# Kernel optimization log

Hardware: AMD Instinct MI355X
Metric: run time of the kernel (lower is better)

The kernel has to match this reference:

```python
import jax, jax.numpy as jnp
import numpy as np

EPS = 1e-5

def layer_norm(x, gamma):
    mu = jnp.mean(x, axis=-1, keepdims=True)
    var = jnp.mean(jnp.square(x - mu), axis=-1, keepdims=True)
    return (x - mu) / jnp.sqrt(var + EPS) * gamma

def setup_inputs() -> dict:
    key = jax.random.key(0)
    ks = jax.random.split(key, 10)
    b, n, j = 2, 2048, 2048
    dim, ctx_dim, heads, dim_head, ff_mult = 1024, 1024, 16, 64, 4
    inner = heads * dim_head
    ff_inner = ff_mult * dim
    s = 0.02
    return {
        'x': jax.random.normal(ks[0], (b, n, dim), jnp.float32),
        'context': jax.random.normal(ks[1], (b, j, ctx_dim), jnp.float32),
        'mask': jax.random.randint(ks[2], (b, j), 0, 2, jnp.int32),
        'gamma': jnp.ones((dim,), jnp.float32),
        'ctx_gamma': jnp.ones((ctx_dim,), jnp.float32),
        'Wq': jax.random.normal(ks[3], (dim, inner), jnp.float32) * s,
        'Wkv': jax.random.normal(ks[4], (ctx_dim, 2 * dim_head), jnp.float32) * s,
        'Wout': jax.random.normal(ks[5], (inner, dim), jnp.float32) * s,
        'Wff1': jax.random.normal(ks[6], (dim, 2 * ff_inner), jnp.float32) * s,
        'Wff2': jax.random.normal(ks[7], (ff_inner, dim), jnp.float32) * s,
    }

def reference(x, context, mask, gamma, ctx_gamma, Wq, Wkv, Wout, Wff1, Wff2):
    heads, dim_head = 16, 64
    b, n, dim = x.shape
    scale = dim_head ** -0.5
    xn = layer_norm(x, gamma)                              # [b,n,dim]
    ctx = layer_norm(context, ctx_gamma)                   # [b,j,cd]
    q = (xn @ Wq).reshape(b, n, heads, dim_head).transpose(0, 2, 1, 3) * scale  # [b,h,n,d]
    kv = ctx @ Wkv                                         # [b,j,2d]
    k, v = kv[..., :dim_head], kv[..., dim_head:]          # [b,j,d] each (multi-query)
    sim = jnp.einsum('bhid,bjd->bhij', q, k)               # [b,h,n,j]
    sim = jnp.where((mask == 0)[:, None, None, :], -jnp.inf, sim)
    attn = jax.nn.softmax(sim, axis=-1)
    out = jnp.einsum('bhij,bjd->bhid', attn, v)            # [b,h,n,d]
    out = out.transpose(0, 2, 1, 3).reshape(b, n, heads * dim_head)
    out = out @ Wout                                       # [b,n,dim]
    # parallel SwiGLU FF on normalized x
    h = xn @ Wff1
    ff_inner = Wff2.shape[0]
    a, gate = h[..., :ff_inner], h[..., ff_inner:]
    out = out + (jax.nn.silu(gate) * a) @ Wff2
    return out
```

## Files before the change

### kernel.cpp

```cpp
#include <hip/hip_runtime.h>

typedef unsigned short u16;
typedef unsigned int   u32;
typedef __bf16  bf16x8 __attribute__((ext_vector_type(8)));
typedef __bf16  bf16x2 __attribute__((ext_vector_type(2)));
typedef float   f32x4  __attribute__((ext_vector_type(4)));

static __device__ __forceinline__ float b2f(u16 v) {
    return __builtin_bit_cast(float, (u32)(((u32)v) << 16));
}
static __device__ __forceinline__ u16 f2b(float f) {
    u32 u = __builtin_bit_cast(u32, f);
    return (u16)((u + 0x7FFFu + ((u >> 16) & 1u)) >> 16);
}
static __device__ __forceinline__ u32 pack2(float a, float b) {
    bf16x2 t; t[0] = (__bf16)a; t[1] = (__bf16)b;
    return __builtin_bit_cast(u32, t);
}

__global__ __launch_bounds__(256)
void ln_kernel(const float* __restrict__ x, const float* __restrict__ ctx,
               const float* __restrict__ gamma, const float* __restrict__ cgamma,
               u16* __restrict__ xn, u16* __restrict__ ctxn)
{
    const int row = blockIdx.x;
    const int tid = threadIdx.x;
    const float* src; const float* g; u16* dst;
    if (row < 4096) { src = x   + (long)row * 1024;          g = gamma;  dst = xn   + (long)row * 1024; }
    else            { src = ctx + (long)(row - 4096) * 1024; g = cgamma; dst = ctxn + (long)(row - 4096) * 1024; }
    float4 v = ((const float4*)src)[tid];
    float s = v.x + v.y + v.z + v.w;
    float q = v.x*v.x + v.y*v.y + v.z*v.z + v.w*v.w;
#pragma unroll
    for (int off = 32; off; off >>= 1) { s += __shfl_xor(s, off); q += __shfl_xor(q, off); }
    __shared__ float r1[4], r2[4];
    if ((tid & 63) == 0) { r1[tid >> 6] = s; r2[tid >> 6] = q; }
    __syncthreads();
    s = r1[0] + r1[1] + r1[2] + r1[3];
    q = r2[0] + r2[1] + r2[2] + r2[3];
    float mu   = s * (1.0f / 1024.0f);
    float var  = q * (1.0f / 1024.0f) - mu * mu;
    float rstd = rsqrtf(var + 1e-5f);
    float4 gv = ((const float4*)g)[tid];
    ushort4 o;
    o.x = f2b((v.x - mu) * rstd * gv.x);
    o.y = f2b((v.y - mu) * rstd * gv.y);
    o.z = f2b((v.z - mu) * rstd * gv.z);
    o.w = f2b((v.w - mu) * rstd * gv.w);
    ((ushort4*)dst)[tid] = o;
}

__global__ __launch_bounds__(256)
void wconv(const float* __restrict__ W, u16* __restrict__ Wt, int N, int K, float scale)
{
    __shared__ float tile[32][33];
    const int tid = threadIdx.x;
    const int n0 = blockIdx.x * 32;
    const int k0 = blockIdx.y * 32;
    const int r  = tid >> 3;
    const int c4 = (tid & 7) * 4;
    float4 v = *(const float4*)&W[(long)(k0 + r) * N + n0 + c4];
    tile[r][c4 + 0] = v.x; tile[r][c4 + 1] = v.y; tile[r][c4 + 2] = v.z; tile[r][c4 + 3] = v.w;
    __syncthreads();
    ushort4 o;
    o.x = f2b(tile[c4 + 0][r] * scale);
    o.y = f2b(tile[c4 + 1][r] * scale);
    o.z = f2b(tile[c4 + 2][r] * scale);
    o.w = f2b(tile[c4 + 3][r] * scale);
    *(ushort4*)&Wt[(long)(n0 + r) * K + k0 + c4] = o;
}

__global__ __launch_bounds__(256)
void wconv_ff1(const float* __restrict__ W, u16* __restrict__ Wt)
{
    __shared__ float tile[32][33];
    const int tid = threadIdx.x;
    const int a  = blockIdx.x;
    const int k0 = blockIdx.y * 32;
    const int r  = tid >> 3;
    const int c4 = (tid & 7) * 4;
    const int srccol = (c4 < 16) ? (a * 16 + c4) : (4096 + a * 16 + (c4 - 16));
    float4 v = *(const float4*)&W[(long)(k0 + r) * 8192 + srccol];
    tile[r][c4 + 0] = v.x; tile[r][c4 + 1] = v.y; tile[r][c4 + 2] = v.z; tile[r][c4 + 3] = v.w;
    __syncthreads();
    ushort4 o;
    o.x = f2b(tile[c4 + 0][r]);
    o.y = f2b(tile[c4 + 1][r]);
    o.z = f2b(tile[c4 + 2][r]);
    o.w = f2b(tile[c4 + 3][r]);
    *(ushort4*)&Wt[(long)(a * 32 + r) * 1024 + k0 + c4] = o;
}

__global__ __launch_bounds__(256)
void kext_build(const float* __restrict__ kvf, const int* __restrict__ mask,
                u16* __restrict__ kext, float* __restrict__ mbias)
{
    const int gid = blockIdx.x * 256 + threadIdx.x;
    const int b = gid >> 14;
    const int rem = gid & 16383;
    const int j = rem >> 3;
    const int c = rem & 7;
    const float* src = &kvf[((long)b * 2048 + j) * 128 + c * 8];
    u16 ov[8];
#pragma unroll
    for (int e = 0; e < 8; ++e) ov[e] = f2b(src[e]);
    uint4 w;
    w.x = (u32)ov[0] | ((u32)ov[1] << 16);
    w.y = (u32)ov[2] | ((u32)ov[3] << 16);
    w.z = (u32)ov[4] | ((u32)ov[5] << 16);
    w.w = (u32)ov[6] | ((u32)ov[7] << 16);
    *(uint4*)&kext[((long)b * 2048 + j) * 64 + c * 8] = w;
    if (c == 0) mbias[b * 2048 + j] = mask[b * 2048 + j] ? 0.0f : -1e30f;
}

__global__ __launch_bounds__(256)
void vtrans(const float* __restrict__ kvf, u16* __restrict__ vT)
{
    const int j = blockIdx.x * 256 + threadIdx.x;
    const int d = blockIdx.y;
    const int b = blockIdx.z;
    vT[(long)b * 64 * 2048 + (long)d * 2048 + j] =
        f2b(kvf[((long)b * 2048 + j) * 128 + 64 + d]);
}

#define BM 128
#define BN 128
#define BK 32

template<int EPI>
__global__ __launch_bounds__(256, 2)
void gemm_bt(const u16* __restrict__ A, const u16* __restrict__ Bt,
             void* __restrict__ Cv,
             int K, int lda, int ldb, int ldc,
             long aH, long bH, long cH)
{
    __shared__ __align__(16) u16 sm[2][2][BM * BK];
    const int tid  = threadIdx.x;
    const int wave = tid >> 6;
    const int lane = tid & 63;
    const int gx = gridDim.x;
    const int nwg = gx * gridDim.y;
    int wg = blockIdx.y * gx + blockIdx.x;
    if ((nwg & 7) == 0 && nwg >= 16)
        wg = (wg & 7) * (nwg >> 3) + (wg >> 3);
    const int tn = (wg % gx) * BN;
    const int tm = (wg / gx) * BM;
    const int z  = blockIdx.z;
    A  += (long)z * aH;
    Bt += (long)z * bH;

    const int arow0 = (tid >> 2);
    const int arow1 = 64 + (tid >> 2);
    const int acs0  = (tid & 3) ^ ((arow0 >> 1) & 3);
    const int acs1  = (tid & 3) ^ ((arow1 >> 1) & 3);
    const int nt = K / BK;

#define STAGE(buf, k0)                                                                              \
    do {                                                                                            \
        __builtin_amdgcn_global_load_lds(                                                           \
            (const __attribute__((address_space(1))) void*)(A + (long)(tm + arow0) * lda + (k0) + acs0 * 8),   \
            (__attribute__((address_space(3))) void*)(&sm[buf][0][(wave * 64) * 8]), 16, 0, 0);     \
        __builtin_amdgcn_global_load_lds(                                                           \
            (const __attribute__((address_space(1))) void*)(A + (long)(tm + arow1) * lda + (k0) + acs1 * 8),   \
            (__attribute__((address_space(3))) void*)(&sm[buf][0][(256 + wave * 64) * 8]), 16, 0, 0); \
        __builtin_amdgcn_global_load_lds(                                                           \
            (const __attribute__((address_space(1))) void*)(Bt + (long)(tn + arow0) * ldb + (k0) + acs0 * 8),  \
            (__attribute__((address_space(3))) void*)(&sm[buf][1][(wave * 64) * 8]), 16, 0, 0);     \
        __builtin_amdgcn_global_load_lds(                                                           \
            (const __attribute__((address_space(1))) void*)(Bt + (long)(tn + arow1) * ldb + (k0) + acs1 * 8),  \
            (__attribute__((address_space(3))) void*)(&sm[buf][1][(256 + wave * 64) * 8]), 16, 0, 0); \
    } while (0)

    STAGE(0, 0);

    f32x4 acc[4][4] = {};
    const int wr   = (wave >> 1) * 64;
    const int wc   = (wave & 1) * 64;
    const int frow = lane & 15;
    const int fk   = lane >> 4;

    for (int t = 0; t < nt; ++t) {
        __syncthreads();
        if (t + 1 < nt) STAGE((t + 1) & 1, (t + 1) * BK);
        const int cur = t & 1;
        bf16x8 af[4], bf[4];
#pragma unroll
        for (int m = 0; m < 4; ++m) {
            int row = wr + m * 16 + frow;
            af[m] = *(const bf16x8*)&sm[cur][0][row * BK + ((fk ^ ((row >> 1) & 3)) * 8)];
        }
#pragma unroll
        for (int n = 0; n < 4; ++n) {
            int row = wc + n * 16 + frow;
            bf[n] = *(const bf16x8*)&sm[cur][1][row * BK + ((fk ^ ((row >> 1) & 3)) * 8)];
        }
#pragma unroll
        for (int m = 0; m < 4; ++m)
#pragma unroll
            for (int n = 0; n < 4; ++n)
                acc[m][n] = __builtin_amdgcn_mfma_f32_16x16x32_bf16(af[m], bf[n], acc[m][n], 0, 0, 0);
    }
#undef STAGE

    const long coff = (long)z * cH;
    if constexpr (EPI == 3) {
#pragma unroll
        for (int m = 0; m < 4; ++m) {
            const int row0 = tm + wr + m * 16 + fk * 4;
#pragma unroll
            for (int np = 0; np < 4; np += 2) {
                const int col = ((tn + wc + np * 16) >> 5) * 16 + frow;
                f32x4 av = acc[m][np], gv = acc[m][np + 1];
#pragma unroll
                for (int r = 0; r < 4; ++r) {
                    const float g = gv[r];
                    const float o = av[r] * g / (1.0f + __expf(-g));
                    ((u16*)Cv)[(long)(row0 + r) * ldc + col] = f2b(o);
                }
            }
        }
    } else {
#pragma unroll
        for (int m = 0; m < 4; ++m) {
            const int row0 = tm + wr + m * 16 + fk * 4;
#pragma unroll
            for (int n = 0; n < 4; ++n) {
                const int col = tn + wc + n * 16 + frow;
#pragma unroll
                for (int r = 0; r < 4; ++r) {
                    const long off = coff + (long)(row0 + r) * ldc + col;
                    const float v = acc[m][n][r];
                    if constexpr (EPI == 0)      ((u16*)Cv)[off] = f2b(v);
                    else if constexpr (EPI == 1) ((float*)Cv)[off] = v;
                    else if constexpr (EPI == 2) ((float*)Cv)[off] += v;
                    else                         atomicAdd(&((float*)Cv)[off], v);
                }
            }
        }
    }
}

__global__ __launch_bounds__(256, 4)
void flash_attn(const u16* __restrict__ qb, const u16* __restrict__ kext,
                const u16* __restrict__ vT, const float* __restrict__ mbias,
                u16* __restrict__ aout)
{
    __shared__ __align__(16) u16 Ksm[2][4096];
    __shared__ __align__(16) u16 Vsm[2][4096];
    __shared__ __align__(16) u16 Psm[4][1024];
    const int tid  = threadIdx.x;
    const int wave = tid >> 6, lane = tid & 63;
    const int frow = lane & 15, fk = lane >> 4;
    const int b = blockIdx.z, h = blockIdx.y;
    const int q0 = blockIdx.x * 64;

    const u16* kx = kext + (long)b * 2048 * 64;
    const u16* vb = vT   + (long)b * 64 * 2048;
    const float* mbb = mbias + b * 2048;

    const u16* qbase = qb + ((long)(b * 2048 + q0 + wave * 16 + frow)) * 1024 + h * 64;
    bf16x8 bq[2];
#pragma unroll
    for (int kk = 0; kk < 2; ++kk)
        bq[kk] = *(const bf16x8*)&qbase[kk * 32 + fk * 8];

#define FSTAGE(buf, j0s)                                                                             \
    do {                                                                                             \
        _Pragma("unroll")                                                                            \
        for (int i = 0; i < 2; ++i) {                                                                \
            const int slot = i * 256 + tid;                                                          \
            const int row  = slot >> 3;                                                              \
            const int csrc = (slot & 7) ^ (row & 7);                                                 \
            __builtin_amdgcn_global_load_lds(                                                        \
                (const __attribute__((address_space(1))) void*)(kx + (long)((j0s) + row) * 64 + csrc * 8), \
                (__attribute__((address_space(3))) void*)(&Ksm[buf][(i * 256 + wave * 64) * 8]), 16, 0, 0); \
            __builtin_amdgcn_global_load_lds(                                                        \
                (const __attribute__((address_space(1))) void*)(vb + (long)row * 2048 + (j0s) + csrc * 8),  \
                (__attribute__((address_space(3))) void*)(&Vsm[buf][(i * 256 + wave * 64) * 8]), 16, 0, 0); \
        }                                                                                            \
    } while (0)

    FSTAGE(0, 0);

    f32x4 oacc[4] = {};
    float mrun = -1e30f, lrun = 0.0f;
    u16* pw = &Psm[wave][0];

    for (int it = 0; it < 32; ++it) {
        const int j0 = it * 64;
        __syncthreads();
        float4 mb[4];
#pragma unroll
        for (int m = 0; m < 4; ++m)
            mb[m] = *(const float4*)&mbb[j0 + m * 16 + fk * 4];
        if (it + 1 < 32) FSTAGE((it + 1) & 1, (it + 1) * 64);
        const int cur = it & 1;

        f32x4 st[4] = {};
        __builtin_amdgcn_s_setprio(1);
#pragma unroll
        for (int kk = 0; kk < 2; ++kk) {
            bf16x8 ka[4];
#pragma unroll
            for (int m = 0; m < 4; ++m) {
                const int row = m * 16 + frow;
                ka[m] = *(const bf16x8*)&Ksm[cur][row * 64 + (((kk * 4 + fk) ^ (row & 7)) * 8)];
            }
#pragma unroll
            for (int m = 0; m < 4; ++m)
                st[m] = __builtin_amdgcn_mfma_f32_16x16x32_bf16(ka[m], bq[kk], st[m], 0, 0, 0);
        }
        __builtin_amdgcn_s_setprio(0);

        float sb[4][4];
#pragma unroll
        for (int m = 0; m < 4; ++m)
#pragma unroll
            for (int r = 0; r < 4; ++r) sb[m][r] = st[m][r] + (&mb[m].x)[r];
        float pm = fmaxf(
            fmaxf(fmaxf(sb[0][0], sb[0][1]), fmaxf(sb[0][2], sb[0][3])),
            fmaxf(fmaxf(sb[1][0], sb[1][1]), fmaxf(sb[1][2], sb[1][3])));
        pm = fmaxf(pm, fmaxf(
            fmaxf(fmaxf(sb[2][0], sb[2][1]), fmaxf(sb[2][2], sb[2][3])),
            fmaxf(fmaxf(sb[3][0], sb[3][1]), fmaxf(sb[3][2], sb[3][3]))));
        pm = fmaxf(pm, __shfl_xor(pm, 16));
        pm = fmaxf(pm, __shfl_xor(pm, 32));
        const float nm = fmaxf(mrun, pm);
        const float alpha = __expf(mrun - nm);
        mrun = nm;

        float rs = 0.0f;
#pragma unroll
        for (int m = 0; m < 4; ++m) {
            const float p0 = __expf(sb[m][0] - nm);
            const float p1 = __expf(sb[m][1] - nm);
            const float p2 = __expf(sb[m][2] - nm);
            const float p3 = __expf(sb[m][3] - nm);
            rs += (p0 + p1) + (p2 + p3);
            const int chunk = (m * 2 + (fk >> 1)) ^ (frow & 7);
            uint2 w; w.x = pack2(p0, p1); w.y = pack2(p2, p3);
            *(uint2*)&pw[frow * 64 + chunk * 8 + (fk & 1) * 4] = w;
        }
        rs += __shfl_xor(rs, 16);
        rs += __shfl_xor(rs, 32);
        lrun = lrun * alpha + rs;
#pragma unroll
        for (int mo = 0; mo < 4; ++mo)
#pragma unroll
            for (int r = 0; r < 4; ++r) oacc[mo][r] *= alpha;

        __builtin_amdgcn_s_setprio(1);
#pragma unroll
        for (int kkv = 0; kkv < 2; ++kkv) {
            bf16x8 va[4];
#pragma unroll
            for (int mo = 0; mo < 4; ++mo) {
                const int row = mo * 16 + frow;
                va[mo] = *(const bf16x8*)&Vsm[cur][row * 64 + (((kkv * 4 + fk) ^ (row & 7)) * 8)];
            }
            const bf16x8 pb = *(const bf16x8*)&pw[frow * 64 + (((kkv * 4 + fk) ^ (frow & 7)) * 8)];
#pragma unroll
            for (int mo = 0; mo < 4; ++mo)
                oacc[mo] = __builtin_amdgcn_mfma_f32_16x16x32_bf16(va[mo], pb, oacc[mo], 0, 0, 0);
        }
        __builtin_amdgcn_s_setprio(0);
    }
#undef FSTAGE

    const float inv = 1.0f / lrun;
    const long row = (long)b * 2048 + q0 + wave * 16 + frow;
#pragma unroll
    for (int mo = 0; mo < 4; ++mo) {
        uint2 w;
        w.x = pack2(oacc[mo][0] * inv, oacc[mo][1] * inv);
        w.y = pack2(oacc[mo][2] * inv, oacc[mo][3] * inv);
        *(uint2*)&aout[row * 1024 + h * 64 + mo * 16 + fk * 4] = w;
    }
}

extern "C" void kernel_launch(void* const* d_in, const int* in_sizes, int n_in,
                              void* d_out, int out_size, void* d_ws, size_t ws_size,
                              hipStream_t stream)
{
    const float* x      = (const float*)d_in[0];
    const float* ctx    = (const float*)d_in[1];
    const int*   mask   = (const int*)d_in[2];
    const float* gamma  = (const float*)d_in[3];
    const float* cgamma = (const float*)d_in[4];
    const float* Wq     = (const float*)d_in[5];
    const float* Wkv    = (const float*)d_in[6];
    const float* Wout   = (const float*)d_in[7];
    const float* Wff1   = (const float*)d_in[8];
    const float* Wff2   = (const float*)d_in[9];
    float* out = (float*)d_out;

    char* w = (char*)d_ws;
    auto carveB = [&](long bytes) { char* p = w; w += ((bytes + 255) / 256) * 256; return p; };
    u16*   xn     = (u16*)  carveB(4096L * 1024 * 2);
    u16*   ctxn   = (u16*)  carveB(4096L * 1024 * 2);
    u16*   WqT    = (u16*)  carveB(1024L * 1024 * 2);
    u16*   WkvT   = (u16*)  carveB(128L * 1024 * 2);
    u16*   WoutT  = (u16*)  carveB(1024L * 1024 * 2);
    u16*   Wff1Tp = (u16*)  carveB(8192L * 1024 * 2);
    u16*   Wff2T  = (u16*)  carveB(1024L * 4096 * 2);
    u16*   q      = (u16*)  carveB(4096L * 1024 * 2);
    float* kvf    = (float*)carveB(2L * 2048 * 128 * 4);
    u16*   kext   = (u16*)  carveB(2L * 2048 * 64 * 2);
    float* mbias  = (float*)carveB(2L * 2048 * 4);
    u16*   vT     = (u16*)  carveB(2L * 64 * 2048 * 2);
    u16*   aout   = (u16*)  carveB(4096L * 1024 * 2);
    u16*   gbuf   = (u16*)  carveB(4096L * 4096 * 2);

    dim3 B(256);

    ln_kernel<<<dim3(8192), B, 0, stream>>>(x, ctx, gamma, cgamma, xn, ctxn);
    wconv<<<dim3(32, 32),  B, 0, stream>>>(Wq,   WqT,   1024, 1024, 0.125f);
    wconv<<<dim3(4, 32),   B, 0, stream>>>(Wkv,  WkvT,  128,  1024, 1.0f);
    wconv<<<dim3(32, 32),  B, 0, stream>>>(Wout, WoutT, 1024, 1024, 1.0f);
    wconv_ff1<<<dim3(256, 32), B, 0, stream>>>(Wff1, Wff1Tp);
    wconv<<<dim3(32, 128), B, 0, stream>>>(Wff2, Wff2T, 1024, 4096, 1.0f);

    gemm_bt<0><<<dim3(8, 32, 1), B, 0, stream>>>(xn, WqT, q, 1024, 1024, 1024, 1024, 0, 0, 0);
    hipMemsetAsync(kvf, 0, 2L * 2048 * 128 * 4, stream);
    gemm_bt<4><<<dim3(1, 32, 4), B, 0, stream>>>(ctxn, WkvT, kvf, 256, 1024, 1024, 128, 256, 256, 0);
    kext_build<<<dim3(128), B, 0, stream>>>(kvf, mask, kext, mbias);
    vtrans<<<dim3(8, 64, 2), B, 0, stream>>>(kvf, vT);

    flash_attn<<<dim3(32, 16, 2), B, 0, stream>>>(q, kext, vT, mbias, aout);

    gemm_bt<1><<<dim3(8, 32, 1), B, 0, stream>>>(aout, WoutT, out, 1024, 1024, 1024, 1024, 0, 0, 0);
    gemm_bt<3><<<dim3(64, 32, 1), B, 0, stream>>>(xn, Wff1Tp, gbuf, 1024, 1024, 1024, 4096, 0, 0, 0);
    gemm_bt<2><<<dim3(8, 32, 1), B, 0, stream>>>(gbuf, Wff2T, out, 4096, 4096, 4096, 1024, 0, 0, 0);
}
```

Measured before the change: 425.0 us.

## Add dedicated 256x256 tiled GEMM kernel for FF1 with fused SwiGLU epilogue

Replaces the 128x128 generic GEMM used for the FF1 projection with a new 512-thread kernel that computes 256x256 output tiles with BK=64, double-buffered direct-to-LDS loads, XOR swizzle and raised wave priority during MFMA. Larger tiles increase operand reuse per LDS load and cut global traffic for this largest GEMM. The SwiGLU epilogue moves into the new kernel. The generic GEMM also drops its grouped workgroup remapping and its EPI==3 path, which may change L2 locality for the remaining GEMMs. The new kernel uses large LDS (128KB) and many accumulator registers, which limits occupancy.

```diff
diff --git a/kernel.cpp b/kernel.cpp
--- a/kernel.cpp
+++ b/kernel.cpp
@@ -138,13 +138,8 @@
     const int tid  = threadIdx.x;
     const int wave = tid >> 6;
     const int lane = tid & 63;
-    const int gx = gridDim.x;
-    const int nwg = gx * gridDim.y;
-    int wg = blockIdx.y * gx + blockIdx.x;
-    if ((nwg & 7) == 0 && nwg >= 16)
-        wg = (wg & 7) * (nwg >> 3) + (wg >> 3);
-    const int tn = (wg % gx) * BN;
-    const int tm = (wg / gx) * BM;
+    const int tn = blockIdx.x * BN;
+    const int tm = blockIdx.y * BM;
     const int z  = blockIdx.z;
     A  += (long)z * aH;
     Bt += (long)z * bH;
@@ -203,38 +198,120 @@
 #undef STAGE
 
     const long coff = (long)z * cH;
-    if constexpr (EPI == 3) {
-#pragma unroll
-        for (int m = 0; m < 4; ++m) {
-            const int row0 = tm + wr + m * 16 + fk * 4;
-#pragma unroll
-            for (int np = 0; np < 4; np += 2) {
-                const int col = ((tn + wc + np * 16) >> 5) * 16 + frow;
-                f32x4 av = acc[m][np], gv = acc[m][np + 1];
-#pragma unroll
-                for (int r = 0; r < 4; ++r) {
-                    const float g = gv[r];
-                    const float o = av[r] * g / (1.0f + __expf(-g));
-                    ((u16*)Cv)[(long)(row0 + r) * ldc + col] = f2b(o);
-                }
+#pragma unroll
+    for (int m = 0; m < 4; ++m) {
+        const int row0 = tm + wr + m * 16 + fk * 4;
+#pragma unroll
+        for (int n = 0; n < 4; ++n) {
+            const int col = tn + wc + n * 16 + frow;
+#pragma unroll
+            for (int r = 0; r < 4; ++r) {
+                const long off = coff + (long)(row0 + r) * ldc + col;
+                const float v = acc[m][n][r];
+                if constexpr (EPI == 0)      ((u16*)Cv)[off] = f2b(v);
+                else if constexpr (EPI == 1) ((float*)Cv)[off] = v;
+                else if constexpr (EPI == 2) ((float*)Cv)[off] += v;
+                else                         atomicAdd(&((float*)Cv)[off], v);
             }
         }
-    } else {
-#pragma unroll
-        for (int m = 0; m < 4; ++m) {
-            const int row0 = tm + wr + m * 16 + fk * 4;
-#pragma unroll
-            for (int n = 0; n < 4; ++n) {
-                const int col = tn + wc + n * 16 + frow;
-#pragma unroll
-                for (int r = 0; r < 4; ++r) {
-                    const long off = coff + (long)(row0 + r) * ldc + col;
-                    const float v = acc[m][n][r];
-                    if constexpr (EPI == 0)      ((u16*)Cv)[off] = f2b(v);
-                    else if constexpr (EPI == 1) ((float*)Cv)[off] = v;
-                    else if constexpr (EPI == 2) ((float*)Cv)[off] += v;
-                    else                         atomicAdd(&((float*)Cv)[off], v);
-                }
+    }
+}
+
+__global__ __launch_bounds__(512, 2)
+void gemm256_ff1(const u16* __restrict__ A, const u16* __restrict__ Bt,
+                 u16* __restrict__ C, int K, int lda, int ldb, int ldc)
+{
+    __shared__ __align__(16) u16 As[2][256 * 64];
+    __shared__ __align__(16) u16 Bs[2][256 * 64];
+    const int tid  = threadIdx.x;
+    const int wave = tid >> 6, lane = tid & 63;
+    const int wm = wave >> 2, wn = wave & 3;
+    const int frow = lane & 15, fk = lane >> 4;
+    const int tn = blockIdx.x * 256;
+    const int tm = blockIdx.y * 256;
+    const int nt = K >> 6;
+
+    int arow[4], acs[4];
+#pragma unroll
+    for (int i = 0; i < 4; ++i) {
+        const int slot = i * 512 + tid;
+        arow[i] = slot >> 3;
+        acs[i]  = ((slot & 7) ^ (arow[i] & 7)) * 8;
+    }
+
+#define STAGE256(buf, k0)                                                                            \
+    do {                                                                                             \
+        _Pragma("unroll")                                                                            \
+        for (int i = 0; i < 4; ++i) {                                                                \
+            __builtin_amdgcn_global_load_lds(                                                        \
+                (const __attribute__((address_space(1))) void*)(A + (long)(tm + arow[i]) * lda + (k0) + acs[i]),  \
+                (__attribute__((address_space(3))) void*)(&As[buf][(i * 512 + wave * 64) * 8]), 16, 0, 0);        \
+            __builtin_amdgcn_global_load_lds(                                                        \
+                (const __attribute__((address_space(1))) void*)(Bt + (long)(tn + arow[i]) * ldb + (k0) + acs[i]), \
+                (__attribute__((address_space(3))) void*)(&Bs[buf][(i * 512 + wave * 64) * 8]), 16, 0, 0);        \
+        }                                                                                            \
+    } while (0)
+
+    STAGE256(0, 0);
+    STAGE256(1, 64);
+    asm volatile("s_waitcnt vmcnt(8)" ::: "memory");
+    __builtin_amdgcn_sched_barrier(0);
+    __builtin_amdgcn_s_barrier();
+
+    f32x4 acc[8][4] = {};
+
+    for (int t = 0; ; ++t) {
+        const int cur = t & 1;
+        const u16* as = &As[cur][0];
+        const u16* bs = &Bs[cur][0];
+#pragma unroll
+        for (int kk = 0; kk < 2; ++kk) {
+            bf16x8 af[8], bfr[4];
+#pragma unroll
+            for (int mf = 0; mf < 8; ++mf) {
+                const int row = wm * 128 + mf * 16 + frow;
+                af[mf] = *(const bf16x8*)&as[row * 64 + (((kk * 4 + fk) ^ (row & 7)) * 8)];
+            }
+#pragma unroll
+            for (int nf = 0; nf < 4; ++nf) {
+                const int row = wn * 64 + nf * 16 + frow;
+                bfr[nf] = *(const bf16x8*)&bs[row * 64 + (((kk * 4 + fk) ^ (row & 7)) * 8)];
+            }
+            __builtin_amdgcn_s_setprio(1);
+#pragma unroll
+            for (int mf = 0; mf < 8; ++mf)
+#pragma unroll
+                for (int nf = 0; nf < 4; ++nf)
+                    acc[mf][nf] = __builtin_amdgcn_mfma_f32_16x16x32_bf16(af[mf], bfr[nf], acc[mf][nf], 0, 0, 0);
+            __builtin_amdgcn_s_setprio(0);
+        }
+        if (t == nt - 1) break;
+        __builtin_amdgcn_sched_barrier(0);
+        __builtin_amdgcn_s_barrier();
+        if (t + 2 < nt) {
+            STAGE256(cur, (t + 2) << 6);
+            asm volatile("s_waitcnt vmcnt(8)" ::: "memory");
+        } else {
+            asm volatile("s_waitcnt vmcnt(0)" ::: "memory");
+        }
+        __builtin_amdgcn_sched_barrier(0);
+        __builtin_amdgcn_s_barrier();
+    }
+#undef STAGE256
+
+#pragma unroll
+    for (int mf = 0; mf < 8; ++mf) {
+        const int gr = tm + wm * 128 + mf * 16 + fk * 4;
+#pragma unroll
+        for (int np = 0; np < 4; np += 2) {
+            const int scol = (tn >> 1) + (wn * 2 + (np >> 1)) * 16 + frow;
+            const f32x4 av = acc[mf][np];
+            const f32x4 gv = acc[mf][np + 1];
+#pragma unroll
+            for (int r = 0; r < 4; ++r) {
+                const float g = gv[r];
+                const float o = av[r] * g / (1.0f + __expf(-g));
+                C[(long)(gr + r) * ldc + scol] = f2b(o);
             }
         }
     }
@@ -429,6 +506,6 @@
     flash_attn<<<dim3(32, 16, 2), B, 0, stream>>>(q, kext, vT, mbias, aout);
 
     gemm_bt<1><<<dim3(8, 32, 1), B, 0, stream>>>(aout, WoutT, out, 1024, 1024, 1024, 1024, 0, 0, 0);
-    gemm_bt<3><<<dim3(64, 32, 1), B, 0, stream>>>(xn, Wff1Tp, gbuf, 1024, 1024, 1024, 4096, 0, 0, 0);
+    gemm256_ff1<<<dim3(32, 16), dim3(512), 0, stream>>>(xn, Wff1Tp, gbuf, 1024, 1024, 1024, 4096);
     gemm_bt<2><<<dim3(8, 32, 1), B, 0, stream>>>(gbuf, Wff2T, out, 4096, 4096, 4096, 1024, 0, 0, 0);
 }
```

Measured after the change: 417.1 us. About the same (-1.9%).
